# Optimization experiments

Measured on AMD Instinct MI355X. Metric: run time of the kernel, lower is better.

## Reference

```python
import jax, jax.numpy as jnp
import numpy as np


def setup_inputs() -> dict:
    key = jax.random.key(0)
    k1, k2 = jax.random.split(key)
    B, T, J, D = 32, 2048, 64, 256
    h = jax.random.normal(k1, (B, T, D), dtype=jnp.float32)
    s = jax.random.normal(k2, (B, T, J), dtype=jnp.float32)
    return {"h": h, "s": s}


def reference(h, s):
    # z1: max similarity over query positions -> [B, T]
    z1 = jnp.max(s, axis=-1)
    # attention over context positions -> [B, T]
    b = jax.nn.softmax(z1, axis=-1)
    # weighted sum of context vectors -> [B, D]
    pooled = jnp.einsum('bt,btd->bd', b, h)
    # tile pooled vector across all T context positions -> [B, T, D]
    q2c = jnp.broadcast_to(pooled[:, None, :], h.shape)
    return q2c
```

## Files before the change

kernel.cpp:

```cpp
#include <hip/hip_runtime.h>
#include <math.h>

#define BQ 32
#define TQ 2048
#define JQ 64
#define DQ 256
#define NBLK 1024
#define NTHR 256


__global__ __launch_bounds__(NTHR) void k_rowmax_exp(
    const float4* __restrict__ s4, float* __restrict__ e,
    float* __restrict__ dpart)
{
    const int blk = blockIdx.x, tid = threadIdx.x;
    __shared__ float e_lds[64];

    #pragma unroll
    for (int p = 0; p < 4; ++p) {
        int idx = blk * 1024 + p * 256 + tid;
        float4 v = s4[idx];
        float m = fmaxf(fmaxf(v.x, v.y), fmaxf(v.z, v.w));
        m = fmaxf(m, __shfl_xor(m, 1));
        m = fmaxf(m, __shfl_xor(m, 2));
        m = fmaxf(m, __shfl_xor(m, 4));
        m = fmaxf(m, __shfl_xor(m, 8));
        if ((tid & 15) == 0)
            e_lds[p * 16 + (tid >> 4)] = expf(m);
    }
    __syncthreads();
    if (tid < 64) {
        float v = e_lds[tid];
        e[blk * 64 + tid] = v;
        #pragma unroll
        for (int off = 32; off > 0; off >>= 1)
            v += __shfl_xor(v, off);
        if (tid == 0) dpart[blk] = v;
    }
}

__global__ __launch_bounds__(NTHR) void k_pool(
    const float4* __restrict__ h4, const float* __restrict__ e,
    const float* __restrict__ dpart, float* __restrict__ ppart)
{
    const int blk = blockIdx.x, tid = threadIdx.x;
    const int b = blk >> 5;

    float den = 0.f;
    #pragma unroll
    for (int c = 0; c < 32; ++c)
        den += dpart[b * 32 + c];
    const float inv = 1.0f / den;

    __shared__ float w_lds[64];
    if (tid < 64) w_lds[tid] = e[blk * 64 + tid] * inv;
    __syncthreads();

    const int t_sub = tid >> 6;
    const int d4 = tid & 63;
    const int t0 = (blk & 31) * 64;
    float4 acc = make_float4(0.f, 0.f, 0.f, 0.f);
    #pragma unroll
    for (int i = 0; i < 16; ++i) {
        int tl = i * 4 + t_sub;
        float wt = w_lds[tl];
        float4 hv = h4[(size_t)(b * TQ + t0 + tl) * (DQ / 4) + d4];
        acc.x += wt * hv.x;
        acc.y += wt * hv.y;
        acc.z += wt * hv.z;
        acc.w += wt * hv.w;
    }

    __shared__ float sred[NTHR][4];
    sred[tid][0] = acc.x; sred[tid][1] = acc.y;
    sred[tid][2] = acc.z; sred[tid][3] = acc.w;
    __syncthreads();
    int dd4 = tid >> 2, c4 = tid & 3;
    float sum = sred[dd4][c4] + sred[64 + dd4][c4] +
                sred[128 + dd4][c4] + sred[192 + dd4][c4];
    ppart[blk * DQ + tid] = sum;
}

__global__ __launch_bounds__(NTHR) void k_reduce_bcast(
    const float* __restrict__ ppart, float4* __restrict__ out4)
{
    const int blk = blockIdx.x, tid = threadIdx.x;
    const int b = blk >> 5;
    __shared__ __align__(16) float pooled[DQ];

    float p = 0.f;
    #pragma unroll
    for (int c = 0; c < 32; ++c)
        p += ppart[(b * 32 + c) * DQ + tid];
    pooled[tid] = p;
    __syncthreads();

    float4 pv = ((const float4*)pooled)[tid & 63];
    size_t base = (size_t)blk * 4096;
    #pragma unroll
    for (int k = 0; k < 16; ++k)
        out4[base + k * 256 + tid] = pv;
}

extern "C" void kernel_launch(void* const* d_in, const int* in_sizes, int n_in,
                              void* d_out, int out_size, void* d_ws, size_t ws_size,
                              hipStream_t stream) {
    const float4* h4 = (const float4*)d_in[0];
    const float4* s4 = (const float4*)d_in[1];
    float4* out4 = (float4*)d_out;

    float* ws = (float*)d_ws;
    float* dpart = ws;
    float* e = ws + NBLK;
    float* ppart = ws + NBLK + BQ * TQ;

    k_rowmax_exp<<<NBLK, NTHR, 0, stream>>>(s4, e, dpart);
    k_pool<<<NBLK, NTHR, 0, stream>>>(h4, e, dpart, ppart);
    k_reduce_bcast<<<NBLK, NTHR, 0, stream>>>(ppart, out4);
}
```

Measured before the change: 131.7 us.

## Fuse row-max/exp into pooling kernel and defer softmax normalization

Merges the row-max/exp kernel and the weighted-pooling kernel into one. Each block now pools h with unnormalized exp weights from shared memory, and the softmax denominator is applied only in the final reduce/broadcast kernel. This removes one kernel launch, the global round trip of the exp array, and the per-block denominator reduction in the pooling stage. The exp values are not max-subtracted, as before, so overflow behaviour is unchanged.

```diff
diff --git a/kernel.cpp b/kernel.cpp
--- a/kernel.cpp
+++ b/kernel.cpp
@@ -9,11 +9,12 @@
 #define NTHR 256
 
 
-__global__ __launch_bounds__(NTHR) void k_rowmax_exp(
-    const float4* __restrict__ s4, float* __restrict__ e,
-    float* __restrict__ dpart)
+__global__ __launch_bounds__(NTHR) void k_fused_pool(
+    const float4* __restrict__ s4, const float4* __restrict__ h4,
+    float* __restrict__ dpart, float* __restrict__ ppart)
 {
     const int blk = blockIdx.x, tid = threadIdx.x;
+    const int b = blk >> 5;
     __shared__ float e_lds[64];
 
     #pragma unroll
@@ -29,32 +30,14 @@
             e_lds[p * 16 + (tid >> 4)] = expf(m);
     }
     __syncthreads();
+
     if (tid < 64) {
         float v = e_lds[tid];
-        e[blk * 64 + tid] = v;
         #pragma unroll
         for (int off = 32; off > 0; off >>= 1)
             v += __shfl_xor(v, off);
         if (tid == 0) dpart[blk] = v;
     }
-}
-
-__global__ __launch_bounds__(NTHR) void k_pool(
-    const float4* __restrict__ h4, const float* __restrict__ e,
-    const float* __restrict__ dpart, float* __restrict__ ppart)
-{
-    const int blk = blockIdx.x, tid = threadIdx.x;
-    const int b = blk >> 5;
-
-    float den = 0.f;
-    #pragma unroll
-    for (int c = 0; c < 32; ++c)
-        den += dpart[b * 32 + c];
-    const float inv = 1.0f / den;
-
-    __shared__ float w_lds[64];
-    if (tid < 64) w_lds[tid] = e[blk * 64 + tid] * inv;
-    __syncthreads();
 
     const int t_sub = tid >> 6;
     const int d4 = tid & 63;
@@ -63,7 +46,7 @@
     #pragma unroll
     for (int i = 0; i < 16; ++i) {
         int tl = i * 4 + t_sub;
-        float wt = w_lds[tl];
+        float wt = e_lds[tl];
         float4 hv = h4[(size_t)(b * TQ + t0 + tl) * (DQ / 4) + d4];
         acc.x += wt * hv.x;
         acc.y += wt * hv.y;
@@ -82,17 +65,24 @@
 }
 
 __global__ __launch_bounds__(NTHR) void k_reduce_bcast(
-    const float* __restrict__ ppart, float4* __restrict__ out4)
+    const float* __restrict__ dpart, const float* __restrict__ ppart,
+    float4* __restrict__ out4)
 {
     const int blk = blockIdx.x, tid = threadIdx.x;
     const int b = blk >> 5;
     __shared__ __align__(16) float pooled[DQ];
 
+    float den = 0.f;
+    #pragma unroll
+    for (int c = 0; c < 32; ++c)
+        den += dpart[b * 32 + c];
+    const float inv = 1.0f / den;
+
     float p = 0.f;
     #pragma unroll
     for (int c = 0; c < 32; ++c)
         p += ppart[(b * 32 + c) * DQ + tid];
-    pooled[tid] = p;
+    pooled[tid] = p * inv;
     __syncthreads();
 
     float4 pv = ((const float4*)pooled)[tid & 63];
@@ -111,10 +101,8 @@
 
     float* ws = (float*)d_ws;
     float* dpart = ws;
-    float* e = ws + NBLK;
-    float* ppart = ws + NBLK + BQ * TQ;
+    float* ppart = ws + NBLK;
 
-    k_rowmax_exp<<<NBLK, NTHR, 0, stream>>>(s4, e, dpart);
-    k_pool<<<NBLK, NTHR, 0, stream>>>(h4, e, dpart, ppart);
-    k_reduce_bcast<<<NBLK, NTHR, 0, stream>>>(ppart, out4);
+    k_fused_pool<<<NBLK, NTHR, 0, stream>>>(s4, h4, dpart, ppart);
+    k_reduce_bcast<<<NBLK, NTHR, 0, stream>>>(dpart, ppart, out4);
 }
```

After: 128.6 us. -2.3%, faster.
